# Performance work log

Hardware: AMD Instinct MI355X
Metric: run time of the kernel (lower is better)

Reference implementation:

```python
import jax, jax.numpy as jnp
import numpy as np

E, H, T_MAX = 1024, 16, 2048
HS = E // H
EPS = 1e-5


def _layernorm(x, g, b):
    m = jnp.mean(x, axis=-1, keepdims=True)
    v = jnp.mean(jnp.square(x - m), axis=-1, keepdims=True)
    return (x - m) * jax.lax.rsqrt(v + EPS) * g + b


def setup_inputs() -> dict:
    key = jax.random.key(0)
    ks = jax.random.split(key, 8)
    B, T = 2, 2048
    s = 0.02
    return {
        "x": jax.random.normal(ks[0], (B, T, E), jnp.float32),
        "ln1_g": jnp.ones((E,), jnp.float32),
        "ln1_b": jnp.zeros((E,), jnp.float32),
        "Wk": jax.random.normal(ks[1], (H, E, HS), jnp.float32) * s,  # stacked per-head key weights (x @ Wk)
        "Wv": jax.random.normal(ks[2], (H, E, HS), jnp.float32) * s,
        "Wproj": jax.random.normal(ks[3], (E, E), jnp.float32) * s,
        "bproj": jnp.zeros((E,), jnp.float32),
        "ln2_g": jnp.ones((E,), jnp.float32),
        "ln2_b": jnp.zeros((E,), jnp.float32),
        "W1": jax.random.normal(ks[4], (E, 4 * E), jnp.float32) * s,
        "b1": jnp.zeros((4 * E,), jnp.float32),
        "W2": jax.random.normal(ks[5], (4 * E, E), jnp.float32) * s,
        "b2": jnp.zeros((E,), jnp.float32),
    }


def reference(x, ln1_g, ln1_b, Wk, Wv, Wproj, bproj, ln2_g, ln2_b, W1, b1, W2, b2):
    B, T, C = x.shape
    h = _layernorm(x, ln1_g, ln1_b)
    # NOTE: original code uses the KEY projection for both q and k (q = self.key(x))
    k = jnp.einsum('bte,hed->bhtd', h, Wk)
    q = k
    wei = jnp.einsum('bhtd,bhsd->bhts', q, k) * (C ** -0.5)  # scale by full n_embd, as in source
    causal = jnp.tril(jnp.ones((T, T), bool))
    wei = jnp.where(causal, wei, -jnp.inf)
    # source applies softmax over dim=1 (the query/row axis of the TxT matrix)
    wei = jax.nn.softmax(wei, axis=2)
    v = jnp.einsum('bte,hed->bhtd', h, Wv)
    attn = jnp.einsum('bhts,bhsd->bhtd', wei, v)          # [B,H,T,HS]
    attn = attn.transpose(0, 2, 1, 3).reshape(B, T, C)    # concat heads
    x = x + attn @ Wproj + bproj
    h2 = _layernorm(x, ln2_g, ln2_b)
    x = x + jax.nn.relu(h2 @ W1 + b1) @ W2 + b2
    return x
```

## Files before the change

### kernel.cpp

```cpp
#include <hip/hip_runtime.h>

using bf16x8 = __attribute__((ext_vector_type(8))) __bf16;
using f32x4  = __attribute__((ext_vector_type(4))) float;

__device__ __forceinline__ f32x4 mfma16(bf16x8 a, bf16x8 b, f32x4 c) {
  return __builtin_amdgcn_mfma_f32_16x16x32_bf16(a, b, c, 0, 0, 0);
}

__device__ __forceinline__ unsigned short f2bf(float f) {
  union { float f; unsigned int u; } x; x.f = f;
  unsigned int u = x.u + 0x7FFFu + ((x.u >> 16) & 1u);
  return (unsigned short)(u >> 16);
}

__device__ __forceinline__ unsigned int cvtpk_bf16(float lo, float hi) {
  unsigned int r;
  asm("v_cvt_pk_bf16_f32 %0, %1, %2" : "=v"(r) : "v"(lo), "v"(hi));
  return r;
}

__device__ __forceinline__ void gl_lds16(const unsigned short* g, unsigned short* l) {
  __builtin_amdgcn_global_load_lds(
      (__attribute__((address_space(1))) void*)(g),
      (__attribute__((address_space(3))) void*)(l), 16, 0, 0);
}

__device__ __forceinline__ bf16x8 rdsw64(const unsigned short* base, int r, int ch) {
  int c = ch ^ (r & 7);
  return *reinterpret_cast<const bf16x8*>(base + ((size_t)r * 8 + c) * 8);
}

__global__ __launch_bounds__(256) void transpose_cvt(const float* __restrict__ in,
                                                     unsigned short* __restrict__ out,
                                                     int R, int C) {
  __shared__ float t[32][33];
  int b = blockIdx.z;
  const float* inb = in + (size_t)b * R * C;
  unsigned short* outb = out + (size_t)b * R * C;
  int tx = threadIdx.x & 31, ty = threadIdx.x >> 5;
  int c0 = blockIdx.x * 32, r0 = blockIdx.y * 32;
#pragma unroll
  for (int i = 0; i < 4; ++i)
    t[ty + i * 8][tx] = inb[(size_t)(r0 + ty + i * 8) * C + c0 + tx];
  __syncthreads();
#pragma unroll
  for (int i = 0; i < 4; ++i)
    outb[(size_t)(c0 + ty + i * 8) * R + r0 + tx] = f2bf(t[tx][ty + i * 8]);
}

__global__ __launch_bounds__(256) void ln_bf16(const float* __restrict__ x,
                                               const float* __restrict__ g,
                                               const float* __restrict__ bta,
                                               unsigned short* __restrict__ out) {
  int row = blockIdx.x, tid = threadIdx.x;
  float4 v = reinterpret_cast<const float4*>(x + (size_t)row * 1024)[tid];
  float s = v.x + v.y + v.z + v.w;
  float s2 = v.x * v.x + v.y * v.y + v.z * v.z + v.w * v.w;
#pragma unroll
  for (int m = 1; m < 64; m <<= 1) { s += __shfl_xor(s, m); s2 += __shfl_xor(s2, m); }
  __shared__ float red[8];
  int w = tid >> 6;
  if ((tid & 63) == 0) { red[w] = s; red[w + 4] = s2; }
  __syncthreads();
  s  = red[0] + red[1] + red[2] + red[3];
  s2 = red[4] + red[5] + red[6] + red[7];
  float mean = s * (1.f / 1024.f);
  float var  = s2 * (1.f / 1024.f) - mean * mean;
  float rstd = rsqrtf(var + 1e-5f);
  float4 gv = reinterpret_cast<const float4*>(g)[tid];
  float4 bv = reinterpret_cast<const float4*>(bta)[tid];
  ushort4 o;
  o.x = f2bf((v.x - mean) * rstd * gv.x + bv.x);
  o.y = f2bf((v.y - mean) * rstd * gv.y + bv.y);
  o.z = f2bf((v.z - mean) * rstd * gv.z + bv.z);
  o.w = f2bf((v.w - mean) * rstd * gv.w + bv.w);
  reinterpret_cast<ushort4*>(out + (size_t)row * 1024)[tid] = o;
}

__device__ __forceinline__ void stage_half(const unsigned short* gbase, int K,
                                           unsigned short* lds, int tid) {
#pragma unroll
  for (int j = 0; j < 2; ++j) {
    int lr = j * 64 + (tid >> 3);
    int c  = (tid & 7) ^ (lr & 7);
    gl_lds16(gbase + (size_t)lr * K + c * 8, lds + (size_t)(j * 512 + tid) * 8);
  }
}

__device__ __forceinline__ bf16x8 rdfrag(const unsigned short* base, int r, int k) {
  return *reinterpret_cast<const bf16x8*>(base + ((size_t)r * 8 + (k ^ (r & 7))) * 8);
}

__global__ __launch_bounds__(512, 2) void gemm256_relu(const unsigned short* __restrict__ A,
                                                       const unsigned short* __restrict__ Bt,
                                                       unsigned short* __restrict__ C,
                                                       const float* __restrict__ bias,
                                                       int M, int N, int K) {
  __shared__ __align__(16) unsigned short LA[2][256 * 64];
  __shared__ __align__(16) unsigned short LB[2][256 * 64];
  int tid = threadIdx.x, lane = tid & 63, w = tid >> 6;
  int l15 = lane & 15, lh = lane >> 4;
  int wr = (w >> 2) * 128, wc = (w & 3) * 64;
  int bid = blockIdx.x;
  int xcd = bid & 7, g = bid >> 3;
  int bm = (xcd >> 1) * 4 + (g >> 3);
  int bn = (xcd & 1) * 8 + (g & 7);
  const unsigned short* Ab = A + (size_t)(bm * 256) * K;
  const unsigned short* Bb = Bt + (size_t)(bn * 256) * K;
  f32x4 acc[8][4] = {};
  int NT = K >> 6;
  stage_half(Ab, K, &LA[0][0], tid);
  stage_half(Ab + (size_t)128 * K, K, &LA[0][128 * 64], tid);
  stage_half(Bb, K, &LB[0][0], tid);
  stage_half(Bb + (size_t)128 * K, K, &LB[0][128 * 64], tid);
  asm volatile("s_waitcnt vmcnt(0)" ::: "memory");
  __builtin_amdgcn_s_barrier();
  for (int t = 0; t < NT; ++t) {
    int cur = t & 1;
    const unsigned short* la = &LA[cur][0];
    const unsigned short* lb = &LB[cur][0];
    unsigned short* na = &LA[cur ^ 1][0];
    unsigned short* nb = &LB[cur ^ 1][0];
    int k0n = (t + 1) << 6;
    bool more = (t + 1 < NT);
    bf16x8 bfr[4][2];
#pragma unroll
    for (int q = 0; q < 4; ++q) {
      if (more) {
        if (q == 0)      stage_half(Ab + k0n, K, na, tid);
        else if (q == 1) stage_half(Ab + (size_t)128 * K + k0n, K, na + 128 * 64, tid);
        else if (q == 2) stage_half(Bb + k0n, K, nb, tid);
        else             stage_half(Bb + (size_t)128 * K + k0n, K, nb + 128 * 64, tid);
      }
      if (q == 0) {
        if (more) asm volatile("s_waitcnt vmcnt(2)" ::: "memory");
        else      asm volatile("s_waitcnt vmcnt(0)" ::: "memory");
        __builtin_amdgcn_s_barrier();
      }
      bf16x8 aq[2][2];
#pragma unroll
      for (int i = 0; i < 2; ++i)
#pragma unroll
        for (int kk = 0; kk < 2; ++kk)
          aq[i][kk] = rdfrag(la, wr + q * 32 + i * 16 + l15, kk * 4 + lh);
      if (q == 0) {
#pragma unroll
        for (int ni = 0; ni < 4; ++ni)
#pragma unroll
          for (int kk = 0; kk < 2; ++kk)
            bfr[ni][kk] = rdfrag(lb, wc + ni * 16 + l15, kk * 4 + lh);
      }
      if (q != 0) __builtin_amdgcn_s_barrier();
      __builtin_amdgcn_s_setprio(1);
#pragma unroll
      for (int kk = 0; kk < 2; ++kk)
#pragma unroll
        for (int i = 0; i < 2; ++i)
#pragma unroll
          for (int ni = 0; ni < 4; ++ni)
            acc[q * 2 + i][ni] = mfma16(aq[i][kk], bfr[ni][kk], acc[q * 2 + i][ni]);
      __builtin_amdgcn_s_setprio(0);
      __builtin_amdgcn_s_barrier();
    }
  }
#pragma unroll
  for (int mi = 0; mi < 8; ++mi)
#pragma unroll
    for (int ni = 0; ni < 4; ++ni) {
      int row0 = bm * 256 + wr + mi * 16 + lh * 4;
      int col  = bn * 256 + wc + ni * 16 + l15;
      float bv = bias[col];
#pragma unroll
      for (int r = 0; r < 4; ++r) {
        float v = fmaxf(acc[mi][ni][r] + bv, 0.f);
        C[(size_t)(row0 + r) * N + col] = f2bf(v);
      }
    }
}

#define GBK 128
#define KSCL 0.04508422f

__device__ __forceinline__ bf16x8 rd128(const unsigned short* base, int r, int ch) {
  int c = ch ^ ((r & 7) << 1);
  return *reinterpret_cast<const bf16x8*>(base + (size_t)r * GBK + c * 8);
}

template<int TM, int MODE>
__global__ __launch_bounds__(256) void gemm_bf16(const unsigned short* __restrict__ A,
                                                 const unsigned short* __restrict__ Bt,
                                                 void* __restrict__ Cout,
                                                 unsigned short* __restrict__ Cout2,
                                                 const float* __restrict__ bias,
                                                 const float* __restrict__ resid,
                                                 const float* __restrict__ scvec,
                                                 int M, int N, int K) {
  constexpr int MI = TM / 32;
  constexpr int AJ = TM / 16;
  __shared__ __align__(16) unsigned short Sh[(TM + 128) * GBK];
  unsigned short* As = Sh;
  unsigned short* Bs = Sh + TM * GBK;
  int tid = threadIdx.x;
  int lane = tid & 63, w = tid >> 6;
  int l15 = lane & 15, lh = lane >> 4;
  int wr = (w >> 1) * (TM / 2), wc = (w & 1) * 64;
  int nblk = N >> 7;
  int rows = M / TM;
  int bm, bn;
  if (nblk == 8 && (rows & 7) == 0) {
    int bid = blockIdx.x;
    int xcd = bid & 7, g = bid >> 3;
    bm = xcd * (rows >> 3) + (g >> 3);
    bn = g & 7;
  } else {
    bm = blockIdx.x / nblk; bn = blockIdx.x % nblk;
  }
  const unsigned short* ApJ[AJ];
  const unsigned short* BpJ[8];
#pragma unroll
  for (int j = 0; j < AJ; ++j) {
    int row = j * 16 + (tid >> 4);
    int ch  = (tid & 15) ^ ((row & 7) << 1);
    ApJ[j] = A + (size_t)(bm * TM + row) * K + ch * 8;
  }
#pragma unroll
  for (int j = 0; j < 8; ++j) {
    int row = j * 16 + (tid >> 4);
    int ch  = (tid & 15) ^ ((row & 7) << 1);
    BpJ[j] = Bt + (size_t)(bn * 128 + row) * K + ch * 8;
  }
  f32x4 acc[MI][4] = {};
  for (int k0 = 0; k0 < K; k0 += GBK) {
#pragma unroll
    for (int j = 0; j < AJ; ++j)
      gl_lds16(ApJ[j] + k0, &As[(j * 256 + tid) * 8]);
#pragma unroll
    for (int j = 0; j < 8; ++j)
      gl_lds16(BpJ[j] + k0, &Bs[(j * 256 + tid) * 8]);
    __syncthreads();
    bf16x8 af[MI][4], bfr[4][4];
#pragma unroll
    for (int i = 0; i < MI; ++i)
#pragma unroll
      for (int kk = 0; kk < 4; ++kk)
        af[i][kk] = rd128(As, wr + i * 16 + l15, kk * 4 + lh);
#pragma unroll
    for (int i = 0; i < 4; ++i)
#pragma unroll
      for (int kk = 0; kk < 4; ++kk)
        bfr[i][kk] = rd128(Bs, wc + i * 16 + l15, kk * 4 + lh);
#pragma unroll
    for (int kk = 0; kk < 4; ++kk)
#pragma unroll
      for (int mi = 0; mi < MI; ++mi)
#pragma unroll
        for (int ni = 0; ni < 4; ++ni)
          acc[mi][ni] = mfma16(af[mi][kk], bfr[ni][kk], acc[mi][ni]);
    __syncthreads();
  }
  if constexpr (MODE == 3) {
#pragma unroll
    for (int mi = 0; mi < MI; ++mi) {
#pragma unroll
      for (int ni = 0; ni < 4; ++ni) {
        int tl = wr + mi * 16 + lh * 4;
        int dl = wc + ni * 16 + l15;
        int colg = bn * 128 + dl;
        int bb = bm >> 5, hh = colg >> 6;
        const float* sp = scvec + (size_t)(bb * 16 + hh) * 2048 + (bm & 31) * 64 + tl;
        float4 rs = *reinterpret_cast<const float4*>(sp);
        unsigned int p0 = f2bf(acc[mi][ni][0] * rs.x) | ((unsigned int)f2bf(acc[mi][ni][1] * rs.y) << 16);
        unsigned int p1 = f2bf(acc[mi][ni][2] * rs.z) | ((unsigned int)f2bf(acc[mi][ni][3] * rs.w) << 16);
        uint2 pk = {p0, p1};
        *reinterpret_cast<uint2*>(&Sh[dl * 64 + (tl ^ ((dl & 7) << 3))]) = pk;
      }
    }
    __syncthreads();
    int dr = tid >> 1, th = (tid & 1) * 32;
    int bb = bm >> 5, tbase = (bm & 31) * 64;
    size_t colg = bn * 128 + dr;
    unsigned short* Vt = (unsigned short*)Cout;
#pragma unroll
    for (int j = 0; j < 4; ++j) {
      int t = th + j * 8;
      int4 v = *reinterpret_cast<const int4*>(&Sh[dr * 64 + (t ^ ((dr & 7) << 3))]);
      *reinterpret_cast<int4*>(&Vt[((size_t)bb * 1024 + colg) * 2048 + tbase + t]) = v;
    }
  } else {
#pragma unroll
    for (int mi = 0; mi < MI; ++mi) {
#pragma unroll
      for (int ni = 0; ni < 4; ++ni) {
        int row0 = bm * TM + wr + mi * 16 + lh * 4;
        int col  = bn * 128 + wc + ni * 16 + l15;
        float bv = (MODE == 2) ? 0.f : bias[col];
#pragma unroll
        for (int r = 0; r < 4; ++r) {
          int row = row0 + r;
          float v = acc[mi][ni][r] + bv;
          if constexpr (MODE == 0) {
            v += resid[(size_t)row * N + col];
            ((float*)Cout)[(size_t)row * N + col] = v;
          } else {
            ((unsigned short*)Cout)[(size_t)row * N + col] = f2bf(v);
            Cout2[(size_t)row * N + col] = f2bf(v * KSCL);
          }
        }
      }
    }
  }
}

__global__ __launch_bounds__(512) void attn_stats(const unsigned short* __restrict__ Kb,
                                                  const unsigned short* __restrict__ Kbs,
                                                  float* __restrict__ colrcp) {
  __shared__ __align__(16) unsigned short Kt[2][64 * 64];
  int bid = blockIdx.x;
  int q = bid >> 8, x = (bid >> 5) & 7, bh = bid & 31;
  int b = bh >> 4, h = bh & 15;
  int sb = q ? (15 - x) : x;
  int tid = threadIdx.x, lane = tid & 63, w = tid >> 6;
  int l15 = lane & 15, lh = lane >> 4;
  int s0 = sb * 128, sw = s0 + w * 16;
  const unsigned short* Kp  = Kb  + ((size_t)b * 2048) * 1024 + h * 64;
  const unsigned short* Kps = Kbs + ((size_t)b * 2048) * 1024 + h * 64;
  bf16x8 as[2];
#pragma unroll
  for (int kc = 0; kc < 2; ++kc)
    as[kc] = *reinterpret_cast<const bf16x8*>(Kp + (size_t)(sw + l15) * 1024 + kc * 32 + (lh << 3));
  int srow = tid >> 3;
  int sch  = (tid & 7) ^ (srow & 7);
  const unsigned short* ksrc = Kps + (size_t)srow * 1024 + sch * 8;
  gl_lds16(ksrc + (size_t)s0 * 1024, &Kt[0][tid * 8]);
  __syncthreads();
  float l[4] = {0.f, 0.f, 0.f, 0.f};
  int nt = 32 - 2 * sb;
  for (int it = 0; it < nt; ++it) {
    int t0 = s0 + it * 64;
    int cur = it & 1;
    if (it + 1 < nt)
      gl_lds16(ksrc + (size_t)(t0 + 64) * 1024, &Kt[cur ^ 1][tid * 8]);
    if (t0 + 63 >= sw) {
      bool dmask = (t0 < sw + 16);
#pragma unroll
      for (int tf = 0; tf < 4; ++tf) {
        int tr = tf * 16 + l15;
        bf16x8 bt0 = rdsw64(&Kt[cur][0], tr, lh);
        bf16x8 bt1 = rdsw64(&Kt[cur][0], tr, 4 + lh);
        f32x4 z = {};
        f32x4 sa = mfma16(as[1], bt1, mfma16(as[0], bt0, z));
        int tg = t0 + tr;
#pragma unroll
        for (int r = 0; r < 4; ++r) {
          float e = exp2f(sa[r]);
          if (dmask) { int sg = sw + lh * 4 + r; e = (tg >= sg) ? e : 0.f; }
          l[r] += e;
        }
      }
    }
    __syncthreads();
  }
#pragma unroll
  for (int m = 1; m < 16; m <<= 1)
#pragma unroll
    for (int r = 0; r < 4; ++r)
      l[r] += __shfl_xor(l[r], m);
  if (l15 == 0) {
#pragma unroll
    for (int r = 0; r < 4; ++r)
      colrcp[(size_t)bh * 2048 + sw + lh * 4 + r] = 1.f / l[r];
  }
}

__global__ __launch_bounds__(512) void attn_pv(const unsigned short* __restrict__ Kb,
                                               const unsigned short* __restrict__ Kbs,
                                               const unsigned short* __restrict__ Vt,
                                               unsigned short* __restrict__ attn) {
  __shared__ __align__(16) unsigned short Ks[2][64 * 64];
  __shared__ __align__(16) unsigned short Vs[2][64 * 64];
  __shared__ __align__(16) unsigned short Pl[8][16][68];
  int bid = blockIdx.x;
  int q = bid >> 8, x = (bid >> 5) & 7, bh = bid & 31;
  int b = bh >> 4, h = bh & 15;
  int tb = q ? (15 - x) : x;
  int tid = threadIdx.x, lane = tid & 63, w = tid >> 6;
  int l15 = lane & 15, lh = lane >> 4;
  int t0 = tb * 128, tw = t0 + w * 16;
  const unsigned short* Kp  = Kb  + ((size_t)b * 2048) * 1024 + h * 64;
  const unsigned short* Kps = Kbs + ((size_t)b * 2048) * 1024 + h * 64;
  const unsigned short* Vp  = Vt + (size_t)bh * 64 * 2048;
  bf16x8 at[2];
#pragma unroll
  for (int kc = 0; kc < 2; ++kc)
    at[kc] = *reinterpret_cast<const bf16x8*>(Kp + (size_t)(tw + l15) * 1024 + kc * 32 + (lh << 3));
  int srow = tid >> 3;
  int sch  = (tid & 7) ^ (srow & 7);
  const unsigned short* ksrc = Kps + (size_t)srow * 1024 + sch * 8;
  const unsigned short* vsrc = Vp + (size_t)srow * 2048 + sch * 8;
  gl_lds16(ksrc, &Ks[0][tid * 8]);
  gl_lds16(vsrc, &Vs[0][tid * 8]);
  __syncthreads();
  f32x4 acc[4] = {};
  int nt = 2 * tb + 2;
  for (int it = 0; it < nt; ++it) {
    int s0 = it * 64;
    int cur = it & 1;
    if (it + 1 < nt) {
      gl_lds16(ksrc + (size_t)(s0 + 64) * 1024, &Ks[cur ^ 1][tid * 8]);
      gl_lds16(vsrc + (s0 + 64), &Vs[cur ^ 1][tid * 8]);
    }
    if (s0 <= tw + 15) {
      bool dmask = (s0 + 63 > tw);
#pragma unroll
      for (int sf = 0; sf < 4; ++sf) {
        int sr = sf * 16 + l15;
        bf16x8 ks0 = rdsw64(&Ks[cur][0], sr, lh);
        bf16x8 ks1 = rdsw64(&Ks[cur][0], sr, 4 + lh);
        f32x4 z = {};
        f32x4 sa = mfma16(ks1, at[1], mfma16(ks0, at[0], z));
        float pe[4];
#pragma unroll
        for (int r = 0; r < 4; ++r) {
          float p = exp2f(sa[r]);
          if (dmask) {
            int sg = s0 + sf * 16 + lh * 4 + r;
            int tg = tw + l15;
            p = (sg <= tg) ? p : 0.f;
          }
          pe[r] = p;
        }
        unsigned int u0 = cvtpk_bf16(pe[0], pe[1]);
        unsigned int u1 = cvtpk_bf16(pe[2], pe[3]);
        unsigned long long pk = (unsigned long long)u0 | ((unsigned long long)u1 << 32);
        *reinterpret_cast<unsigned long long*>(&Pl[w][l15][sf * 16 + lh * 4]) = pk;
      }
#pragma unroll
      for (int c2 = 0; c2 < 2; ++c2) {
        bf16x8 pa = *reinterpret_cast<const bf16x8*>(&Pl[w][l15][c2 * 32 + (lh << 3)]);
#pragma unroll
        for (int nf = 0; nf < 4; ++nf) {
          int dr = nf * 16 + l15;
          bf16x8 vb = rdsw64(&Vs[cur][0], dr, c2 * 4 + lh);
          acc[nf] = mfma16(pa, vb, acc[nf]);
        }
      }
    }
    __syncthreads();
  }
#pragma unroll
  for (int nf = 0; nf < 4; ++nf)
#pragma unroll
    for (int r = 0; r < 4; ++r) {
      int t = tw + lh * 4 + r;
      attn[(size_t)(b * 2048 + t) * 1024 + h * 64 + nf * 16 + l15] = f2bf(acc[nf][r]);
    }
}

extern "C" void kernel_launch(void* const* d_in, const int* in_sizes, int n_in,
                              void* d_out, int out_size, void* d_ws, size_t ws_size,
                              hipStream_t stream) {
  (void)in_sizes; (void)n_in; (void)out_size; (void)ws_size;
  const float* x     = (const float*)d_in[0];
  const float* ln1_g = (const float*)d_in[1];
  const float* ln1_b = (const float*)d_in[2];
  const float* Wk    = (const float*)d_in[3];
  const float* Wv    = (const float*)d_in[4];
  const float* Wproj = (const float*)d_in[5];
  const float* bproj = (const float*)d_in[6];
  const float* ln2_g = (const float*)d_in[7];
  const float* ln2_b = (const float*)d_in[8];
  const float* W1    = (const float*)d_in[9];
  const float* b1    = (const float*)d_in[10];
  const float* W2    = (const float*)d_in[11];
  const float* b2    = (const float*)d_in[12];
  float* out = (float*)d_out;

  char* ws = (char*)d_ws;
  size_t off = 0;
  auto alloc = [&](size_t bytes) { void* p = ws + off; off += (bytes + 255) & ~(size_t)255; return p; };
  unsigned short* bufA = (unsigned short*)alloc((size_t)4096 * 1024 * 2);
  unsigned short* wk_t = (unsigned short*)alloc((size_t)1024 * 1024 * 2);
  unsigned short* wv_t = (unsigned short*)alloc((size_t)1024 * 1024 * 2);
  unsigned short* wp_t = (unsigned short*)alloc((size_t)1024 * 1024 * 2);
  unsigned short* w1_t = (unsigned short*)alloc((size_t)1024 * 4096 * 2);
  unsigned short* w2_t = (unsigned short*)alloc((size_t)4096 * 1024 * 2);
  unsigned short* Kb   = (unsigned short*)alloc((size_t)4096 * 1024 * 2);
  unsigned short* Kbs  = (unsigned short*)alloc((size_t)4096 * 1024 * 2);
  unsigned short* Vt   = (unsigned short*)alloc((size_t)4096 * 1024 * 2);
  float* colrcp = (float*)alloc((size_t)32 * 2048 * 4);
  float* y      = (float*)alloc((size_t)4096 * 1024 * 4);
  unsigned short* act = (unsigned short*)alloc((size_t)4096 * 4096 * 2);

  dim3 b256(256), b512(512);
  transpose_cvt<<<dim3(2, 32, 16), b256, 0, stream>>>(Wk, wk_t, 1024, 64);
  transpose_cvt<<<dim3(2, 32, 16), b256, 0, stream>>>(Wv, wv_t, 1024, 64);
  transpose_cvt<<<dim3(32, 32, 1), b256, 0, stream>>>(Wproj, wp_t, 1024, 1024);
  transpose_cvt<<<dim3(128, 32, 1), b256, 0, stream>>>(W1, w1_t, 1024, 4096);
  transpose_cvt<<<dim3(32, 128, 1), b256, 0, stream>>>(W2, w2_t, 4096, 1024);

  ln_bf16<<<4096, b256, 0, stream>>>(x, ln1_g, ln1_b, bufA);
  gemm_bf16<64, 2><<<512, b256, 0, stream>>>(bufA, wk_t, Kb, Kbs, nullptr, nullptr, nullptr, 4096, 1024, 1024);
  attn_stats<<<512, b512, 0, stream>>>(Kb, Kbs, colrcp);
  gemm_bf16<64, 3><<<512, b256, 0, stream>>>(bufA, wv_t, Vt, nullptr, nullptr, nullptr, colrcp, 4096, 1024, 1024);
  attn_pv<<<512, b512, 0, stream>>>(Kb, Kbs, Vt, bufA);
  gemm_bf16<64, 0><<<512, b256, 0, stream>>>(bufA, wp_t, y, nullptr, bproj, x, nullptr, 4096, 1024, 1024);
  ln_bf16<<<4096, b256, 0, stream>>>(y, ln2_g, ln2_b, bufA);
  gemm256_relu<<<256, dim3(512), 0, stream>>>(bufA, w1_t, act, b1, 4096, 4096, 1024);
  gemm_bf16<64, 0><<<512, b256, 0, stream>>>(act, w2_t, out, nullptr, b2, y, nullptr, 4096, 1024, 4096);
}
```

Measured before the change: 252.2 us.

## Triple-buffer K/V tiles in attention kernels with finer-grained vmcnt waits

Both attention kernels move from double to triple buffering of the K (and V) LDS tiles, prefetching two tiles ahead. The full __syncthreads is replaced by explicit s_waitcnt vmcnt counts plus a raw s_barrier, so each iteration waits only for the tile it is about to use. In attn_pv, the PV MFMA section is also raised in wave priority with s_setprio. The aim is to hide more global-load latency, at the cost of extra LDS, which may reduce occupancy. The hand-managed wait counts also risk races if the compiler emits other vector memory ops in between.

```diff
diff --git a/kernel.cpp b/kernel.cpp
--- a/kernel.cpp
+++ b/kernel.cpp
@@ -314,7 +314,7 @@
 __global__ __launch_bounds__(512) void attn_stats(const unsigned short* __restrict__ Kb,
                                                   const unsigned short* __restrict__ Kbs,
                                                   float* __restrict__ colrcp) {
-  __shared__ __align__(16) unsigned short Kt[2][64 * 64];
+  __shared__ __align__(16) unsigned short Kt[3][64 * 64];
   int bid = blockIdx.x;
   int q = bid >> 8, x = (bid >> 5) & 7, bh = bid & 31;
   int b = bh >> 4, h = bh & 15;
@@ -331,15 +331,18 @@
   int srow = tid >> 3;
   int sch  = (tid & 7) ^ (srow & 7);
   const unsigned short* ksrc = Kps + (size_t)srow * 1024 + sch * 8;
+  int nt = 32 - 2 * sb;
   gl_lds16(ksrc + (size_t)s0 * 1024, &Kt[0][tid * 8]);
-  __syncthreads();
+  gl_lds16(ksrc + (size_t)(s0 + 64) * 1024, &Kt[1][tid * 8]);
+  asm volatile("s_waitcnt vmcnt(1)" ::: "memory");
+  __builtin_amdgcn_s_barrier();
   float l[4] = {0.f, 0.f, 0.f, 0.f};
-  int nt = 32 - 2 * sb;
   for (int it = 0; it < nt; ++it) {
     int t0 = s0 + it * 64;
-    int cur = it & 1;
-    if (it + 1 < nt)
-      gl_lds16(ksrc + (size_t)(t0 + 64) * 1024, &Kt[cur ^ 1][tid * 8]);
+    int cur = it % 3;
+    bool iss = (it + 2 < nt);
+    if (iss)
+      gl_lds16(ksrc + (size_t)(t0 + 128) * 1024, &Kt[(it + 2) % 3][tid * 8]);
     if (t0 + 63 >= sw) {
       bool dmask = (t0 < sw + 16);
 #pragma unroll
@@ -358,7 +361,11 @@
         }
       }
     }
-    __syncthreads();
+    if (it + 1 < nt) {
+      if (iss) asm volatile("s_waitcnt vmcnt(1)" ::: "memory");
+      else     asm volatile("s_waitcnt vmcnt(0)" ::: "memory");
+      __builtin_amdgcn_s_barrier();
+    }
   }
 #pragma unroll
   for (int m = 1; m < 16; m <<= 1)
@@ -376,8 +383,8 @@
                                                const unsigned short* __restrict__ Kbs,
                                                const unsigned short* __restrict__ Vt,
                                                unsigned short* __restrict__ attn) {
-  __shared__ __align__(16) unsigned short Ks[2][64 * 64];
-  __shared__ __align__(16) unsigned short Vs[2][64 * 64];
+  __shared__ __align__(16) unsigned short Ks[3][64 * 64];
+  __shared__ __align__(16) unsigned short Vs[3][64 * 64];
   __shared__ __align__(16) unsigned short Pl[8][16][68];
   int bid = blockIdx.x;
   int q = bid >> 8, x = (bid >> 5) & 7, bh = bid & 31;
@@ -397,17 +404,22 @@
   int sch  = (tid & 7) ^ (srow & 7);
   const unsigned short* ksrc = Kps + (size_t)srow * 1024 + sch * 8;
   const unsigned short* vsrc = Vp + (size_t)srow * 2048 + sch * 8;
+  int nt = 2 * tb + 2;
   gl_lds16(ksrc, &Ks[0][tid * 8]);
   gl_lds16(vsrc, &Vs[0][tid * 8]);
-  __syncthreads();
+  gl_lds16(ksrc + (size_t)64 * 1024, &Ks[1][tid * 8]);
+  gl_lds16(vsrc + 64, &Vs[1][tid * 8]);
+  asm volatile("s_waitcnt vmcnt(2)" ::: "memory");
+  __builtin_amdgcn_s_barrier();
   f32x4 acc[4] = {};
-  int nt = 2 * tb + 2;
   for (int it = 0; it < nt; ++it) {
     int s0 = it * 64;
-    int cur = it & 1;
-    if (it + 1 < nt) {
-      gl_lds16(ksrc + (size_t)(s0 + 64) * 1024, &Ks[cur ^ 1][tid * 8]);
-      gl_lds16(vsrc + (s0 + 64), &Vs[cur ^ 1][tid * 8]);
+    int cur = it % 3;
+    bool iss = (it + 2 < nt);
+    if (iss) {
+      int nb = (it + 2) % 3;
+      gl_lds16(ksrc + (size_t)(s0 + 128) * 1024, &Ks[nb][tid * 8]);
+      gl_lds16(vsrc + (s0 + 128), &Vs[nb][tid * 8]);
     }
     if (s0 <= tw + 15) {
       bool dmask = (s0 + 63 > tw);
@@ -434,6 +446,7 @@
         unsigned long long pk = (unsigned long long)u0 | ((unsigned long long)u1 << 32);
         *reinterpret_cast<unsigned long long*>(&Pl[w][l15][sf * 16 + lh * 4]) = pk;
       }
+      __builtin_amdgcn_s_setprio(1);
 #pragma unroll
       for (int c2 = 0; c2 < 2; ++c2) {
         bf16x8 pa = *reinterpret_cast<const bf16x8*>(&Pl[w][l15][c2 * 32 + (lh << 3)]);
@@ -444,8 +457,13 @@
           acc[nf] = mfma16(pa, vb, acc[nf]);
         }
       }
-    }
-    __syncthreads();
+      __builtin_amdgcn_s_setprio(0);
+    }
+    if (it + 1 < nt) {
+      if (iss) asm volatile("s_waitcnt vmcnt(2)" ::: "memory");
+      else     asm volatile("s_waitcnt vmcnt(0)" ::: "memory");
+      __builtin_amdgcn_s_barrier();
+    }
   }
 #pragma unroll
   for (int nf = 0; nf < 4; ++nf)
```

Measured after the change: 252.7 us. About the same (+0.2%).

## Rewrite attention kernels as per-wave strips reading K/V directly from global

Applied to the files above, without the earlier changes.

Both attention kernels drop the LDS double-buffered tiles shared by 8 waves and instead give each wave a 16-row strip, paired across waves (g, 63-g, 64+g, 127-g) to balance causal work. Each wave loads K and V fragments straight from global memory through the caches, with no block-level syncs, and the causal mask is applied only on the diagonal tile. The launch changes to 1024 blocks of 256 threads, and exp2f is replaced with the raw hardware exp instruction. This removes barriers and skipped-tile idle time, but every wave now refetches K and V from L2 with no LDS reuse across waves.

```diff
diff --git a/kernel.cpp b/kernel.cpp
--- a/kernel.cpp
+++ b/kernel.cpp
@@ -19,15 +19,18 @@
   return r;
 }
 
+__device__ __forceinline__ float fexp2(float x) {
+#if __has_builtin(__builtin_amdgcn_exp2f)
+  return __builtin_amdgcn_exp2f(x);
+#else
+  float r; asm("v_exp_f32 %0, %1" : "=v"(r) : "v"(x)); return r;
+#endif
+}
+
 __device__ __forceinline__ void gl_lds16(const unsigned short* g, unsigned short* l) {
   __builtin_amdgcn_global_load_lds(
       (__attribute__((address_space(1))) void*)(g),
       (__attribute__((address_space(3))) void*)(l), 16, 0, 0);
-}
-
-__device__ __forceinline__ bf16x8 rdsw64(const unsigned short* base, int r, int ch) {
-  int c = ch ^ (r & 7);
-  return *reinterpret_cast<const bf16x8*>(base + ((size_t)r * 8 + c) * 8);
 }
 
 __global__ __launch_bounds__(256) void transpose_cvt(const float* __restrict__ in,
@@ -311,54 +314,42 @@
   }
 }
 
-__global__ __launch_bounds__(512) void attn_stats(const unsigned short* __restrict__ Kb,
+__global__ __launch_bounds__(256) void attn_stats(const unsigned short* __restrict__ Kb,
                                                   const unsigned short* __restrict__ Kbs,
                                                   float* __restrict__ colrcp) {
-  __shared__ __align__(16) unsigned short Kt[2][64 * 64];
   int bid = blockIdx.x;
-  int q = bid >> 8, x = (bid >> 5) & 7, bh = bid & 31;
+  int bh = bid & 31, g = bid >> 5;
   int b = bh >> 4, h = bh & 15;
-  int sb = q ? (15 - x) : x;
   int tid = threadIdx.x, lane = tid & 63, w = tid >> 6;
   int l15 = lane & 15, lh = lane >> 4;
-  int s0 = sb * 128, sw = s0 + w * 16;
+  int strip = (w == 0) ? g : (w == 1) ? 63 - g : (w == 2) ? 64 + g : 127 - g;
+  int sw = strip * 16;
   const unsigned short* Kp  = Kb  + ((size_t)b * 2048) * 1024 + h * 64;
   const unsigned short* Kps = Kbs + ((size_t)b * 2048) * 1024 + h * 64;
-  bf16x8 as[2];
-#pragma unroll
-  for (int kc = 0; kc < 2; ++kc)
-    as[kc] = *reinterpret_cast<const bf16x8*>(Kp + (size_t)(sw + l15) * 1024 + kc * 32 + (lh << 3));
-  int srow = tid >> 3;
-  int sch  = (tid & 7) ^ (srow & 7);
-  const unsigned short* ksrc = Kps + (size_t)srow * 1024 + sch * 8;
-  gl_lds16(ksrc + (size_t)s0 * 1024, &Kt[0][tid * 8]);
-  __syncthreads();
+  bf16x8 as0 = *reinterpret_cast<const bf16x8*>(Kp + (size_t)(sw + l15) * 1024 + (lh << 3));
+  bf16x8 as1 = *reinterpret_cast<const bf16x8*>(Kp + (size_t)(sw + l15) * 1024 + 32 + (lh << 3));
   float l[4] = {0.f, 0.f, 0.f, 0.f};
-  int nt = 32 - 2 * sb;
-  for (int it = 0; it < nt; ++it) {
-    int t0 = s0 + it * 64;
-    int cur = it & 1;
-    if (it + 1 < nt)
-      gl_lds16(ksrc + (size_t)(t0 + 64) * 1024, &Kt[cur ^ 1][tid * 8]);
-    if (t0 + 63 >= sw) {
-      bool dmask = (t0 < sw + 16);
-#pragma unroll
-      for (int tf = 0; tf < 4; ++tf) {
-        int tr = tf * 16 + l15;
-        bf16x8 bt0 = rdsw64(&Kt[cur][0], tr, lh);
-        bf16x8 bt1 = rdsw64(&Kt[cur][0], tr, 4 + lh);
-        f32x4 z = {};
-        f32x4 sa = mfma16(as[1], bt1, mfma16(as[0], bt0, z));
-        int tg = t0 + tr;
-#pragma unroll
-        for (int r = 0; r < 4; ++r) {
-          float e = exp2f(sa[r]);
-          if (dmask) { int sg = sw + lh * 4 + r; e = (tg >= sg) ? e : 0.f; }
-          l[r] += e;
-        }
-      }
-    }
-    __syncthreads();
+  int iters = 128 - strip;
+  {
+    const unsigned short* tp = Kps + (size_t)(sw + l15) * 1024;
+    bf16x8 bt0 = *reinterpret_cast<const bf16x8*>(tp + (lh << 3));
+    bf16x8 bt1 = *reinterpret_cast<const bf16x8*>(tp + 32 + (lh << 3));
+    f32x4 z = {};
+    f32x4 sa = mfma16(as1, bt1, mfma16(as0, bt0, z));
+#pragma unroll
+    for (int r = 0; r < 4; ++r)
+      l[r] += (l15 >= lh * 4 + r) ? fexp2(sa[r]) : 0.f;
+  }
+#pragma unroll 2
+  for (int i = 1; i < iters; ++i) {
+    const unsigned short* tp = Kps + (size_t)(sw + i * 16 + l15) * 1024;
+    bf16x8 bt0 = *reinterpret_cast<const bf16x8*>(tp + (lh << 3));
+    bf16x8 bt1 = *reinterpret_cast<const bf16x8*>(tp + 32 + (lh << 3));
+    f32x4 z = {};
+    f32x4 sa = mfma16(as1, bt1, mfma16(as0, bt0, z));
+#pragma unroll
+    for (int r = 0; r < 4; ++r)
+      l[r] += fexp2(sa[r]);
   }
 #pragma unroll
   for (int m = 1; m < 16; m <<= 1)
@@ -372,80 +363,96 @@
   }
 }
 
-__global__ __launch_bounds__(512) void attn_pv(const unsigned short* __restrict__ Kb,
+__global__ __launch_bounds__(256) void attn_pv(const unsigned short* __restrict__ Kb,
                                                const unsigned short* __restrict__ Kbs,
                                                const unsigned short* __restrict__ Vt,
                                                unsigned short* __restrict__ attn) {
-  __shared__ __align__(16) unsigned short Ks[2][64 * 64];
-  __shared__ __align__(16) unsigned short Vs[2][64 * 64];
-  __shared__ __align__(16) unsigned short Pl[8][16][68];
+  __shared__ __align__(16) unsigned short Pl[4][16][68];
   int bid = blockIdx.x;
-  int q = bid >> 8, x = (bid >> 5) & 7, bh = bid & 31;
+  int bh = bid & 31, g = bid >> 5;
   int b = bh >> 4, h = bh & 15;
-  int tb = q ? (15 - x) : x;
   int tid = threadIdx.x, lane = tid & 63, w = tid >> 6;
   int l15 = lane & 15, lh = lane >> 4;
-  int t0 = tb * 128, tw = t0 + w * 16;
+  int strip = (w == 0) ? g : (w == 1) ? 63 - g : (w == 2) ? 64 + g : 127 - g;
+  int tw = strip * 16;
   const unsigned short* Kp  = Kb  + ((size_t)b * 2048) * 1024 + h * 64;
   const unsigned short* Kps = Kbs + ((size_t)b * 2048) * 1024 + h * 64;
   const unsigned short* Vp  = Vt + (size_t)bh * 64 * 2048;
-  bf16x8 at[2];
-#pragma unroll
-  for (int kc = 0; kc < 2; ++kc)
-    at[kc] = *reinterpret_cast<const bf16x8*>(Kp + (size_t)(tw + l15) * 1024 + kc * 32 + (lh << 3));
-  int srow = tid >> 3;
-  int sch  = (tid & 7) ^ (srow & 7);
-  const unsigned short* ksrc = Kps + (size_t)srow * 1024 + sch * 8;
-  const unsigned short* vsrc = Vp + (size_t)srow * 2048 + sch * 8;
-  gl_lds16(ksrc, &Ks[0][tid * 8]);
-  gl_lds16(vsrc, &Vs[0][tid * 8]);
-  __syncthreads();
+  bf16x8 at0 = *reinterpret_cast<const bf16x8*>(Kp + (size_t)(tw + l15) * 1024 + (lh << 3));
+  bf16x8 at1 = *reinterpret_cast<const bf16x8*>(Kp + (size_t)(tw + l15) * 1024 + 32 + (lh << 3));
   f32x4 acc[4] = {};
-  int nt = 2 * tb + 2;
-  for (int it = 0; it < nt; ++it) {
-    int s0 = it * 64;
-    int cur = it & 1;
-    if (it + 1 < nt) {
-      gl_lds16(ksrc + (size_t)(s0 + 64) * 1024, &Ks[cur ^ 1][tid * 8]);
-      gl_lds16(vsrc + (s0 + 64), &Vs[cur ^ 1][tid * 8]);
-    }
-    if (s0 <= tw + 15) {
-      bool dmask = (s0 + 63 > tw);
-#pragma unroll
-      for (int sf = 0; sf < 4; ++sf) {
-        int sr = sf * 16 + l15;
-        bf16x8 ks0 = rdsw64(&Ks[cur][0], sr, lh);
-        bf16x8 ks1 = rdsw64(&Ks[cur][0], sr, 4 + lh);
-        f32x4 z = {};
-        f32x4 sa = mfma16(ks1, at[1], mfma16(ks0, at[0], z));
-        float pe[4];
-#pragma unroll
-        for (int r = 0; r < 4; ++r) {
-          float p = exp2f(sa[r]);
-          if (dmask) {
-            int sg = s0 + sf * 16 + lh * 4 + r;
-            int tg = tw + l15;
-            p = (sg <= tg) ? p : 0.f;
-          }
-          pe[r] = p;
-        }
-        unsigned int u0 = cvtpk_bf16(pe[0], pe[1]);
-        unsigned int u1 = cvtpk_bf16(pe[2], pe[3]);
-        unsigned long long pk = (unsigned long long)u0 | ((unsigned long long)u1 << 32);
-        *reinterpret_cast<unsigned long long*>(&Pl[w][l15][sf * 16 + lh * 4]) = pk;
-      }
-#pragma unroll
-      for (int c2 = 0; c2 < 2; ++c2) {
-        bf16x8 pa = *reinterpret_cast<const bf16x8*>(&Pl[w][l15][c2 * 32 + (lh << 3)]);
-#pragma unroll
-        for (int nf = 0; nf < 4; ++nf) {
-          int dr = nf * 16 + l15;
-          bf16x8 vb = rdsw64(&Vs[cur][0], dr, c2 * 4 + lh);
-          acc[nf] = mfma16(pa, vb, acc[nf]);
-        }
-      }
-    }
-    __syncthreads();
+  int iters = (strip >> 1) + 1;
+  bool odd = strip & 1;
+  for (int i = 0; i + 1 < iters; ++i) {
+    int s0 = i * 32;
+#pragma unroll
+    for (int st = 0; st < 2; ++st) {
+      const unsigned short* sp = Kps + (size_t)(s0 + st * 16 + l15) * 1024;
+      bf16x8 k0 = *reinterpret_cast<const bf16x8*>(sp + (lh << 3));
+      bf16x8 k1 = *reinterpret_cast<const bf16x8*>(sp + 32 + (lh << 3));
+      f32x4 z = {};
+      f32x4 sa = mfma16(k0, at0, z);
+      sa = mfma16(k1, at1, sa);
+      unsigned int u0 = cvtpk_bf16(fexp2(sa[0]), fexp2(sa[1]));
+      unsigned int u1 = cvtpk_bf16(fexp2(sa[2]), fexp2(sa[3]));
+      unsigned long long pk = (unsigned long long)u0 | ((unsigned long long)u1 << 32);
+      *reinterpret_cast<unsigned long long*>(&Pl[w][l15][st * 16 + lh * 4]) = pk;
+    }
+    bf16x8 pa = *reinterpret_cast<const bf16x8*>(&Pl[w][l15][lh << 3]);
+#pragma unroll
+    for (int nf = 0; nf < 4; ++nf) {
+      bf16x8 vb = *reinterpret_cast<const bf16x8*>(Vp + (size_t)(nf * 16 + l15) * 2048 + s0 + (lh << 3));
+      acc[nf] = mfma16(pa, vb, acc[nf]);
+    }
+  }
+  {
+    int s0 = (iters - 1) * 32;
+    {
+      const unsigned short* sp = Kps + (size_t)(s0 + l15) * 1024;
+      bf16x8 k0 = *reinterpret_cast<const bf16x8*>(sp + (lh << 3));
+      bf16x8 k1 = *reinterpret_cast<const bf16x8*>(sp + 32 + (lh << 3));
+      f32x4 z = {};
+      f32x4 sa = mfma16(k0, at0, z);
+      sa = mfma16(k1, at1, sa);
+      float pe[4];
+      if (!odd) {
+#pragma unroll
+        for (int r = 0; r < 4; ++r)
+          pe[r] = (lh * 4 + r <= l15) ? fexp2(sa[r]) : 0.f;
+      } else {
+#pragma unroll
+        for (int r = 0; r < 4; ++r)
+          pe[r] = fexp2(sa[r]);
+      }
+      unsigned int u0 = cvtpk_bf16(pe[0], pe[1]);
+      unsigned int u1 = cvtpk_bf16(pe[2], pe[3]);
+      unsigned long long pk = (unsigned long long)u0 | ((unsigned long long)u1 << 32);
+      *reinterpret_cast<unsigned long long*>(&Pl[w][l15][lh * 4]) = pk;
+    }
+    if (odd) {
+      const unsigned short* sp = Kps + (size_t)(s0 + 16 + l15) * 1024;
+      bf16x8 k0 = *reinterpret_cast<const bf16x8*>(sp + (lh << 3));
+      bf16x8 k1 = *reinterpret_cast<const bf16x8*>(sp + 32 + (lh << 3));
+      f32x4 z = {};
+      f32x4 sa = mfma16(k0, at0, z);
+      sa = mfma16(k1, at1, sa);
+      float pe[4];
+#pragma unroll
+      for (int r = 0; r < 4; ++r)
+        pe[r] = (lh * 4 + r <= l15) ? fexp2(sa[r]) : 0.f;
+      unsigned int u0 = cvtpk_bf16(pe[0], pe[1]);
+      unsigned int u1 = cvtpk_bf16(pe[2], pe[3]);
+      unsigned long long pk = (unsigned long long)u0 | ((unsigned long long)u1 << 32);
+      *reinterpret_cast<unsigned long long*>(&Pl[w][l15][16 + lh * 4]) = pk;
+    } else {
+      *reinterpret_cast<unsigned long long*>(&Pl[w][l15][16 + lh * 4]) = 0ull;
+    }
+    bf16x8 pa = *reinterpret_cast<const bf16x8*>(&Pl[w][l15][lh << 3]);
+#pragma unroll
+    for (int nf = 0; nf < 4; ++nf) {
+      bf16x8 vb = *reinterpret_cast<const bf16x8*>(Vp + (size_t)(nf * 16 + l15) * 2048 + s0 + (lh << 3));
+      acc[nf] = mfma16(pa, vb, acc[nf]);
+    }
   }
 #pragma unroll
   for (int nf = 0; nf < 4; ++nf)
@@ -491,7 +498,7 @@
   float* y      = (float*)alloc((size_t)4096 * 1024 * 4);
   unsigned short* act = (unsigned short*)alloc((size_t)4096 * 4096 * 2);
 
-  dim3 b256(256), b512(512);
+  dim3 b256(256);
   transpose_cvt<<<dim3(2, 32, 16), b256, 0, stream>>>(Wk, wk_t, 1024, 64);
   transpose_cvt<<<dim3(2, 32, 16), b256, 0, stream>>>(Wv, wv_t, 1024, 64);
   transpose_cvt<<<dim3(32, 32, 1), b256, 0, stream>>>(Wproj, wp_t, 1024, 1024);
@@ -500,9 +507,9 @@
 
   ln_bf16<<<4096, b256, 0, stream>>>(x, ln1_g, ln1_b, bufA);
   gemm_bf16<64, 2><<<512, b256, 0, stream>>>(bufA, wk_t, Kb, Kbs, nullptr, nullptr, nullptr, 4096, 1024, 1024);
-  attn_stats<<<512, b512, 0, stream>>>(Kb, Kbs, colrcp);
+  attn_stats<<<1024, b256, 0, stream>>>(Kb, Kbs, colrcp);
   gemm_bf16<64, 3><<<512, b256, 0, stream>>>(bufA, wv_t, Vt, nullptr, nullptr, nullptr, colrcp, 4096, 1024, 1024);
-  attn_pv<<<512, b512, 0, stream>>>(Kb, Kbs, Vt, bufA);
+  attn_pv<<<1024, b256, 0, stream>>>(Kb, Kbs, Vt, bufA);
   gemm_bf16<64, 0><<<512, b256, 0, stream>>>(bufA, wp_t, y, nullptr, bproj, x, nullptr, 4096, 1024, 1024);
   ln_bf16<<<4096, b256, 0, stream>>>(y, ln2_g, ln2_b, bufA);
   gemm256_relu<<<256, dim3(512), 0, stream>>>(bufA, w1_t, act, b1, 4096, 4096, 1024);
```

New measurement: 351.1 us. 39.2% more time.
